# Kernel optimization log

Measured on AMD Instinct MI355X. Metric: run time of the kernel, lower is better.

Reference implementation:

```python
import jax, jax.numpy as jnp
import numpy as np
from jax import lax

B, S, MAXW, D, V, L = 32, 1024, 256, 512, 32000, 2


def setup_inputs() -> dict:
    key = jax.random.key(0)
    ks = jax.random.split(key, 10)
    x = jax.random.randint(ks[0], (B, S), 0, V)
    labels = jax.random.randint(ks[1], (B, MAXW), 0, 2)
    token_word_id = jnp.sort(
        jax.random.randint(ks[2], (B, S), 0, MAXW), axis=-1
    ).astype(jnp.int32)
    s = 1.0 / np.sqrt(D).astype(np.float32)
    emb = (jax.random.normal(ks[3], (V, D), dtype=jnp.float32) * 0.02).at[0].set(0.0)
    W_ih = jax.random.uniform(ks[4], (L, 4 * D, D), minval=-s, maxval=s, dtype=jnp.float32)
    W_hh = jax.random.uniform(ks[5], (L, 4 * D, D), minval=-s, maxval=s, dtype=jnp.float32)
    b_ih = jax.random.uniform(ks[6], (L, 4 * D), minval=-s, maxval=s, dtype=jnp.float32)
    b_hh = jax.random.uniform(ks[7], (L, 4 * D), minval=-s, maxval=s, dtype=jnp.float32)
    W_out = jax.random.uniform(ks[8], (2, D), minval=-s, maxval=s, dtype=jnp.float32)
    b_out = jax.random.uniform(ks[9], (2,), minval=-s, maxval=s, dtype=jnp.float32)
    return dict(x=x, labels=labels, token_word_id=token_word_id, emb=emb,
                W_ih=W_ih, W_hh=W_hh, b_ih=b_ih, b_hh=b_hh,
                W_out=W_out, b_out=b_out)


def _lstm_layer(xs, Wih, Whh, bih, bhh):
    # xs: [B, S, Din]; torch gate order: i, f, g, o
    H = Whh.shape[1]
    x_proj = jnp.einsum('bsd,gd->bsg', xs, Wih) + bih + bhh  # [B,S,4H]
    h0 = jnp.zeros((xs.shape[0], H), xs.dtype)
    c0 = jnp.zeros((xs.shape[0], H), xs.dtype)

    def step(carry, xt):
        h, c = carry
        gates = xt + h @ Whh.T
        i, f, g, o = jnp.split(gates, 4, axis=-1)
        i = jax.nn.sigmoid(i)
        f = jax.nn.sigmoid(f)
        g = jnp.tanh(g)
        o = jax.nn.sigmoid(o)
        c = f * c + i * g
        h = o * jnp.tanh(c)
        return (h, c), h

    _, hs = lax.scan(step, (h0, c0), x_proj.transpose(1, 0, 2))  # [S,B,H]
    return hs.transpose(1, 0, 2)


def reference(x, labels, token_word_id, emb, W_ih, W_hh, b_ih, b_hh, W_out, b_out):
    h = emb[x]  # [B,S,D]
    for l in range(L):
        h = _lstm_layer(h, W_ih[l], W_hh[l], b_ih[l], b_hh[l])
    # ragged token->word mean pooling (segment mean over flattened batch*word ids)
    seg = (jnp.arange(B, dtype=jnp.int32)[:, None] * MAXW + token_word_id).reshape(-1)
    flat = h.reshape(B * S, D)
    sums = jax.ops.segment_sum(flat, seg, num_segments=B * MAXW)
    cnts = jax.ops.segment_sum(jnp.ones((B * S,), h.dtype), seg, num_segments=B * MAXW)
    pooled = jnp.where(cnts[:, None] > 0, sums / jnp.maximum(cnts, 1.0)[:, None], 0.0)
    # span head (dropout is identity in eval)
    logits = pooled @ W_out.T + b_out            # [B*MAXW, 2]
    logp = jax.nn.log_softmax(logits, axis=-1)
    lab = labels.reshape(-1)
    loss = -jnp.mean(jnp.take_along_axis(logp, lab[:, None], axis=1))
    return logits, loss
```

## Files before the change

kernel.cpp:

```cpp
#include <hip/hip_runtime.h>
#include <hip/hip_fp16.h>

typedef unsigned short u16;
typedef unsigned int u32;
typedef unsigned long long u64;
typedef short s16x8 __attribute__((ext_vector_type(8)));
typedef float f32x4 __attribute__((ext_vector_type(4)));

#define BB   32
#define SS   1024
#define DD   512
#define G4   2048
#define MAXW 256
#define NWG  32
#define RING 8
#define HS   (BB*DD)

__device__ __forceinline__ u16 f2bf(float f){
  unsigned int u = __float_as_uint(f);
  u += 0x7fff + ((u >> 16) & 1);
  return (u16)(u >> 16);
}
__device__ __forceinline__ float bf2f(u16 h){
  return __uint_as_float(((unsigned int)h) << 16);
}
__device__ __forceinline__ float sigm(float x){ return 1.f/(1.f + __expf(-x)); }
__device__ __forceinline__ float ftanh(float x){
  float ax = fabsf(x);
  float e = __expf(-2.f*ax);
  float t = (1.f - e)/(1.f + e);
  return copysignf(t, x);
}

__global__ void k_prep(const float* __restrict__ Wih, const float* __restrict__ Whh,
                       const float* __restrict__ bih, const float* __restrict__ bhh,
                       u16* __restrict__ Wih_b, u16* __restrict__ Whh_b,
                       float* __restrict__ biasp){
  long i = (long)blockIdx.x*blockDim.x + threadIdx.x;
  long n = 2l*G4*DD;
  long stride = (long)gridDim.x*blockDim.x;
  for (long k = i; k < n; k += stride){
    Wih_b[k] = f2bf(Wih[k]);
    Whh_b[k] = f2bf(Whh[k]);
  }
  for (long k = i; k < 2*G4; k += stride){
    int lyr = (int)(k / G4), nn = (int)(k % G4);
    int col = nn >> 2, q = nn & 3;
    int g = q*DD + col;
    biasp[k] = bih[lyr*G4 + g] + bhh[lyr*G4 + g];
  }
}

__global__ void k_embed(const int* __restrict__ x, const float* __restrict__ emb,
                        u16* __restrict__ out){
  int bs = blockIdx.x;
  int tok = x[bs];
  const float* src = emb + (size_t)tok * DD;
  u16* dst = out + (size_t)bs * DD;
  for (int d = threadIdx.x; d < DD; d += blockDim.x) dst[d] = f2bf(src[d]);
}

__device__ __forceinline__ void wait2(const u32* p1, u32 n1,
                                      const u32* p2, u32 n2, int& budget){
  if (n1 == 0u && n2 == 0u) return;
  while (budget > 0){
    u32 v1 = n1 ? __hip_atomic_load(p1, __ATOMIC_RELAXED, __HIP_MEMORY_SCOPE_AGENT)
                : 0xffffffffu;
    u32 v2 = n2 ? __hip_atomic_load(p2, __ATOMIC_RELAXED, __HIP_MEMORY_SCOPE_AGENT)
                : 0xffffffffu;
    int ok = (v1 >= n1) && (v2 >= n2);
    if (__all(ok)) break;
    budget--;
    __builtin_amdgcn_s_sleep(1);
  }
}

__device__ __forceinline__ void stage_h(const u16* slab, char* lds, int tid){
  u64 d[16];
  #pragma unroll
  for (int j = 0; j < 16; j++)
    d[j] = __hip_atomic_load((const u64*)slab + j*256 + tid,
                             __ATOMIC_RELAXED, __HIP_MEMORY_SCOPE_AGENT);
  #pragma unroll
  for (int j = 0; j < 16; j++){
    int e = j*256 + tid;
    int b = e >> 7, c8 = e & 127;
    *(u64*)(lds + b*1024 + ((c8*8) ^ ((b & 7) << 4))) = d[j];
  }
}

#define FRAG_BYT(kk) ((lane & 15)*1024 + (((kk)*64 + (lane>>4)*16) ^ (((lane & 15) & 7) << 4)))

__global__ __launch_bounds__(256, 1) void k_recur2(
    const u16* __restrict__ h_io,
    const u16* __restrict__ Wih_b,
    const u16* __restrict__ Whh_b,
    const float* __restrict__ biasp,
    u16* __restrict__ h1r,
    u16* __restrict__ h2r,
    u32* __restrict__ flags,
    u16* __restrict__ h_seq2){
  __shared__ char hX[32768];
  __shared__ char hH[32768];
  const int tid = threadIdx.x;
  const int lane = tid & 63, wv = tid >> 6;
  const int wg = blockIdx.x;
  const bool isL2 = wg >= NWG;
  const int id = wg & (NWG - 1);

  u32* c1 = flags;
  u32* c2 = flags + 64;

  const int pa = id*64 + wv*16 + (lane & 15);
  const size_t arow = (size_t)((pa & 3)*DD + (pa >> 2))*DD;
  const int koff = (lane >> 4)*8;
  const size_t lyrOff = isL2 ? (size_t)G4*DD : 0;
  s16x8 ahh[16], aih[16];
  #pragma unroll
  for (int kk = 0; kk < 16; kk++){
    ahh[kk] = *(const s16x8*)(Whh_b + lyrOff + arow + kk*32 + koff);
    aih[kk] = *(const s16x8*)(Wih_b + lyrOff + arow + kk*32 + koff);
  }
  #pragma unroll
  for (int kk = 0; kk < 16; kk++){
    asm volatile("" : "+v"(ahh[kk]));
    asm volatile("" : "+v"(aih[kk]));
  }

  const int oc = id*16 + wv*4 + (lane >> 4);
  const int b0 = lane & 15, b1 = b0 + 16;
  const f32x4 b4 = *(const f32x4*)(biasp + (isL2 ? G4 : 0) + oc*4);
  float c0 = 0.f, cst1 = 0.f;
  int budget = 1 << 22;

  if (!isL2){
    for (int t = 0; t < SS; t++){
      u64 xd[16];
      #pragma unroll
      for (int j = 0; j < 16; j++){
        int e = j*256 + tid;
        xd[j] = *((const u64*)h_io + ((size_t)(e >> 7)*SS + t)*128 + (e & 127));
      }
      #pragma unroll
      for (int j = 0; j < 16; j++){
        int e = j*256 + tid;
        int b = e >> 7, c8 = e & 127;
        *(u64*)(hX + b*1024 + ((c8*8) ^ ((b & 7) << 4))) = xd[j];
      }
      __syncthreads();
      f32x4 e0 = {0.f,0.f,0.f,0.f}, e1 = {0.f,0.f,0.f,0.f};
      #pragma unroll
      for (int kk = 0; kk < 16; kk++){
        int byt = FRAG_BYT(kk);
        s16x8 f0 = *(const s16x8*)(hX + byt);
        s16x8 f1 = *(const s16x8*)(hX + byt + 16*1024);
        e0 = __builtin_amdgcn_mfma_f32_16x16x32_bf16(aih[kk], f0, e0, 0, 0, 0);
        e1 = __builtin_amdgcn_mfma_f32_16x16x32_bf16(aih[kk], f1, e1, 0, 0, 0);
      }
      u32 n1 = (t > 0) ? (u32)(NWG*t) : 0u;
      u32 n2 = (t >= RING) ? (u32)(NWG*(t - RING + 1)) : 0u;
      wait2(c1, n1, c2, n2, budget);
      if (t > 0){
        stage_h(h1r + (size_t)((t-1) & (RING-1))*HS, hH, tid);
        __syncthreads();
        #pragma unroll
        for (int kk = 0; kk < 16; kk++){
          int byt = FRAG_BYT(kk);
          s16x8 f0 = *(const s16x8*)(hH + byt);
          s16x8 f1 = *(const s16x8*)(hH + byt + 16*1024);
          e0 = __builtin_amdgcn_mfma_f32_16x16x32_bf16(ahh[kk], f0, e0, 0, 0, 0);
          e1 = __builtin_amdgcn_mfma_f32_16x16x32_bf16(ahh[kk], f1, e1, 0, 0, 0);
        }
      }
      float ig = sigm (e0[0] + b4[0]), fg = sigm (e0[1] + b4[1]);
      float gg = ftanh(e0[2] + b4[2]), og = sigm (e0[3] + b4[3]);
      c0 = fg*c0 + ig*gg;
      float hv0 = og * ftanh(c0);
      ig = sigm (e1[0] + b4[0]); fg = sigm (e1[1] + b4[1]);
      gg = ftanh(e1[2] + b4[2]); og = sigm (e1[3] + b4[3]);
      cst1 = fg*cst1 + ig*gg;
      float hv1 = og * ftanh(cst1);
      u16 hh0 = f2bf(hv0), hh1 = f2bf(hv1);
      u32 p0 = (u32)hh0 | (((u32)__shfl((int)hh0, (lane + 16) & 63) & 0xffffu) << 16);
      u32 p1 = (u32)hh1 | (((u32)__shfl((int)hh1, (lane + 16) & 63) & 0xffffu) << 16);
      u16* dst = h1r + (size_t)(t & (RING-1))*HS;
      if (((lane >> 4) & 1) == 0){
        __hip_atomic_store((u32*)(dst + (size_t)b0*DD + oc), p0,
                           __ATOMIC_RELAXED, __HIP_MEMORY_SCOPE_AGENT);
        __hip_atomic_store((u32*)(dst + (size_t)b1*DD + oc), p1,
                           __ATOMIC_RELAXED, __HIP_MEMORY_SCOPE_AGENT);
      }
      asm volatile("s_waitcnt vmcnt(0)" ::: "memory");
      __syncthreads();
      if (tid == 0) atomicAdd(c1, 1u);
    }
  } else {
    for (int t = 0; t < SS; t++){
      f32x4 e0 = {0.f,0.f,0.f,0.f}, e1 = {0.f,0.f,0.f,0.f};
      if (t > 0){
        wait2(c2, (u32)(NWG*t), c2, 0u, budget);
        stage_h(h2r + (size_t)((t-1) & 1)*HS, hH, tid);
        __syncthreads();
        #pragma unroll
        for (int kk = 0; kk < 16; kk++){
          int byt = FRAG_BYT(kk);
          s16x8 f0 = *(const s16x8*)(hH + byt);
          s16x8 f1 = *(const s16x8*)(hH + byt + 16*1024);
          e0 = __builtin_amdgcn_mfma_f32_16x16x32_bf16(ahh[kk], f0, e0, 0, 0, 0);
          e1 = __builtin_amdgcn_mfma_f32_16x16x32_bf16(ahh[kk], f1, e1, 0, 0, 0);
        }
      }
      wait2(c1, (u32)(NWG*(t+1)), c2, 0u, budget);
      stage_h(h1r + (size_t)(t & (RING-1))*HS, hX, tid);
      __syncthreads();
      #pragma unroll
      for (int kk = 0; kk < 16; kk++){
        int byt = FRAG_BYT(kk);
        s16x8 f0 = *(const s16x8*)(hX + byt);
        s16x8 f1 = *(const s16x8*)(hX + byt + 16*1024);
        e0 = __builtin_amdgcn_mfma_f32_16x16x32_bf16(aih[kk], f0, e0, 0, 0, 0);
        e1 = __builtin_amdgcn_mfma_f32_16x16x32_bf16(aih[kk], f1, e1, 0, 0, 0);
      }
      float ig = sigm (e0[0] + b4[0]), fg = sigm (e0[1] + b4[1]);
      float gg = ftanh(e0[2] + b4[2]), og = sigm (e0[3] + b4[3]);
      c0 = fg*c0 + ig*gg;
      float hv0 = og * ftanh(c0);
      ig = sigm (e1[0] + b4[0]); fg = sigm (e1[1] + b4[1]);
      gg = ftanh(e1[2] + b4[2]); og = sigm (e1[3] + b4[3]);
      cst1 = fg*cst1 + ig*gg;
      float hv1 = og * ftanh(cst1);
      u16 hh0 = f2bf(hv0), hh1 = f2bf(hv1);
      u32 p0 = (u32)hh0 | (((u32)__shfl((int)hh0, (lane + 16) & 63) & 0xffffu) << 16);
      u32 p1 = (u32)hh1 | (((u32)__shfl((int)hh1, (lane + 16) & 63) & 0xffffu) << 16);
      u16* dst = h2r + (size_t)(t & 1)*HS;
      if (((lane >> 4) & 1) == 0){
        __hip_atomic_store((u32*)(dst + (size_t)b0*DD + oc), p0,
                           __ATOMIC_RELAXED, __HIP_MEMORY_SCOPE_AGENT);
        __hip_atomic_store((u32*)(dst + (size_t)b1*DD + oc), p1,
                           __ATOMIC_RELAXED, __HIP_MEMORY_SCOPE_AGENT);
        *(u32*)(h_seq2 + ((size_t)b0*SS + t)*DD + oc) = p0;
        *(u32*)(h_seq2 + ((size_t)b1*SS + t)*DD + oc) = p1;
      }
      asm volatile("s_waitcnt vmcnt(0)" ::: "memory");
      __syncthreads();
      if (tid == 0) atomicAdd(c2, 1u);
    }
  }
}

__global__ __launch_bounds__(64) void k_pool(const u16* __restrict__ h_seq,
                                             const int* __restrict__ twid,
                                             const float* __restrict__ Wout,
                                             const float* __restrict__ bout,
                                             float* __restrict__ out){
  int bw = blockIdx.x;
  int b = bw >> 8, w = bw & 255;
  const int* tw = twid + b*SS;
  __shared__ int s_lo, s_hi;
  if (threadIdx.x == 0){
    int l = 0, r = SS;
    while (l < r){ int m = (l + r) >> 1; if (tw[m] < w) l = m + 1; else r = m; }
    s_lo = l;
    r = SS;
    while (l < r){ int m = (l + r) >> 1; if (tw[m] < w + 1) l = m + 1; else r = m; }
    s_hi = l;
  }
  __syncthreads();
  int lo = s_lo, hi = s_hi, cnt = hi - lo;
  int lane = threadIdx.x;
  float p0 = 0.f, p1 = 0.f;
  if (cnt > 0){
    float sum[8] = {0.f,0.f,0.f,0.f,0.f,0.f,0.f,0.f};
    for (int t = lo; t < hi; t++){
      const u16* hp = h_seq + ((size_t)b*SS + t)*DD + lane*8;
      int4 v = *(const int4*)hp;
      const u16* u = (const u16*)&v;
      #pragma unroll
      for (int j = 0; j < 8; j++) sum[j] += bf2f(u[j]);
    }
    float inv = 1.f/(float)cnt;
    #pragma unroll
    for (int j = 0; j < 8; j++){
      float pv = sum[j]*inv;
      int d = lane*8 + j;
      p0 += pv * Wout[d];
      p1 += pv * Wout[DD + d];
    }
  }
  #pragma unroll
  for (int off = 32; off; off >>= 1){
    p0 += __shfl_down(p0, off);
    p1 += __shfl_down(p1, off);
  }
  if (lane == 0){
    out[bw*2 + 0] = p0 + bout[0];
    out[bw*2 + 1] = p1 + bout[1];
  }
}

__global__ __launch_bounds__(256) void k_loss(const float* __restrict__ logits,
                                              const int* __restrict__ labels,
                                              float* __restrict__ out_loss){
  __shared__ float red[256];
  float acc = 0.f;
  for (int i = threadIdx.x; i < BB*MAXW; i += 256){
    float z0 = logits[i*2], z1 = logits[i*2 + 1];
    float m = fmaxf(z0, z1);
    float lse = m + __logf(__expf(z0 - m) + __expf(z1 - m));
    float zl = labels[i] ? z1 : z0;
    acc += (lse - zl);
  }
  red[threadIdx.x] = acc;
  __syncthreads();
  for (int s2 = 128; s2; s2 >>= 1){
    if (threadIdx.x < s2) red[threadIdx.x] += red[threadIdx.x + s2];
    __syncthreads();
  }
  if (threadIdx.x == 0) out_loss[0] = red[0] / (float)(BB*MAXW);
}

extern "C" void kernel_launch(void* const* d_in, const int* in_sizes, int n_in,
                              void* d_out, int out_size, void* d_ws, size_t ws_size,
                              hipStream_t stream){
  (void)in_sizes; (void)n_in; (void)out_size; (void)ws_size;
  const int*   x      = (const int*)  d_in[0];
  const int*   labels = (const int*)  d_in[1];
  const int*   twid   = (const int*)  d_in[2];
  const float* emb    = (const float*)d_in[3];
  const float* Wih    = (const float*)d_in[4];
  const float* Whh    = (const float*)d_in[5];
  const float* bih    = (const float*)d_in[6];
  const float* bhh    = (const float*)d_in[7];
  const float* Wout   = (const float*)d_in[8];
  const float* bout   = (const float*)d_in[9];
  float* out = (float*)d_out;

  char* ws = (char*)d_ws;
  size_t off = 0;
  u16*   h_io   = (u16*)  (ws + off); off += (size_t)BB*SS*DD*2;
  u16*   h_seq2 = (u16*)  (ws + off); off += (size_t)BB*SS*DD*2;
  u16*   Wih_b  = (u16*)  (ws + off); off += (size_t)2*G4*DD*2;
  u16*   Whh_b  = (u16*)  (ws + off); off += (size_t)2*G4*DD*2;
  float* biasp  = (float*)(ws + off); off += (size_t)2*G4*4;
  u16*   h1r    = (u16*)  (ws + off); off += (size_t)RING*HS*2;
  u16*   h2r    = (u16*)  (ws + off); off += (size_t)2*HS*2;
  u32*   flags  = (u32*)  (ws + off); off += 1024;

  k_prep<<<2048, 256, 0, stream>>>(Wih, Whh, bih, bhh, Wih_b, Whh_b, biasp);
  k_embed<<<BB*SS, 256, 0, stream>>>(x, emb, h_io);

  hipMemsetAsync(flags, 0, 1024, stream);

  k_recur2<<<2*NWG, 256, 0, stream>>>(h_io, Wih_b, Whh_b, biasp,
                                      h1r, h2r, flags, h_seq2);

  k_pool<<<BB*MAXW, 64, 0, stream>>>(h_seq2, twid, Wout, bout, out);
  k_loss<<<1, 256, 0, stream>>>(out, labels, out + BB*MAXW*2);
}
```

Baseline: 5.183 ms.

## Halve LSTM workgroups, double threads, tile hidden-state exchange layout and prefetch inputs

```diff
diff --git a/kernel.cpp b/kernel.cpp
--- a/kernel.cpp
+++ b/kernel.cpp
@@ -12,7 +12,7 @@
 #define DD   512
 #define G4   2048
 #define MAXW 256
-#define NWG  32
+#define NWG  16
 #define RING 8
 #define HS   (BB*DD)
 
@@ -75,23 +75,25 @@
   }
 }
 
-__device__ __forceinline__ void stage_h(const u16* slab, char* lds, int tid){
-  u64 d[16];
-  #pragma unroll
-  for (int j = 0; j < 16; j++)
-    d[j] = __hip_atomic_load((const u64*)slab + j*256 + tid,
+__device__ __forceinline__ void stage_tiled(const u16* slab, char* lds, int tid){
+  u64 d[8];
+  #pragma unroll
+  for (int j = 0; j < 8; j++)
+    d[j] = __hip_atomic_load((const u64*)slab + j*512 + tid,
                              __ATOMIC_RELAXED, __HIP_MEMORY_SCOPE_AGENT);
   #pragma unroll
-  for (int j = 0; j < 16; j++){
-    int e = j*256 + tid;
-    int b = e >> 7, c8 = e & 127;
-    *(u64*)(lds + b*1024 + ((c8*8) ^ ((b & 7) << 4))) = d[j];
+  for (int j = 0; j < 8; j++){
+    int e = j*512 + tid;
+    int tile = e >> 7, u = e & 127;
+    int b = u >> 2, c4 = u & 3;
+    int byt = tile*32 + c4*8;
+    *(u64*)(lds + b*1024 + (byt ^ ((b & 7) << 4))) = d[j];
   }
 }
 
 #define FRAG_BYT(kk) ((lane & 15)*1024 + (((kk)*64 + (lane>>4)*16) ^ (((lane & 15) & 7) << 4)))
 
-__global__ __launch_bounds__(256, 1) void k_recur2(
+__global__ __launch_bounds__(512, 1) void k_recur2(
     const u16* __restrict__ h_io,
     const u16* __restrict__ Wih_b,
     const u16* __restrict__ Whh_b,
@@ -111,7 +113,7 @@
   u32* c1 = flags;
   u32* c2 = flags + 64;
 
-  const int pa = id*64 + wv*16 + (lane & 15);
+  const int pa = id*128 + wv*16 + (lane & 15);
   const size_t arow = (size_t)((pa & 3)*DD + (pa >> 2))*DD;
   const int koff = (lane >> 4)*8;
   const size_t lyrOff = isL2 ? (size_t)G4*DD : 0;
@@ -127,23 +129,28 @@
     asm volatile("" : "+v"(aih[kk]));
   }
 
-  const int oc = id*16 + wv*4 + (lane >> 4);
+  const int oc = id*32 + wv*4 + (lane >> 4);
+  const int cl = wv*4 + (lane >> 4);
   const int b0 = lane & 15, b1 = b0 + 16;
   const f32x4 b4 = *(const f32x4*)(biasp + (isL2 ? G4 : 0) + oc*4);
   float c0 = 0.f, cst1 = 0.f;
   int budget = 1 << 22;
 
+  const int pk_tile = tid >> 8, pk_b = (tid >> 3) & 31, pk_cp = tid & 7;
+  const int pk_lds = pk_b*64 + pk_tile*32 + pk_cp*4;
+  const int pk_word = (id*2 + pk_tile)*256 + pk_b*8 + pk_cp;
+
   if (!isL2){
+    u64 xd[8];
+    #pragma unroll
+    for (int j = 0; j < 8; j++){
+      int e = j*512 + tid;
+      xd[j] = *((const u64*)h_io + ((size_t)(e >> 7)*SS + 0)*128 + (e & 127));
+    }
     for (int t = 0; t < SS; t++){
-      u64 xd[16];
       #pragma unroll
-      for (int j = 0; j < 16; j++){
-        int e = j*256 + tid;
-        xd[j] = *((const u64*)h_io + ((size_t)(e >> 7)*SS + t)*128 + (e & 127));
-      }
-      #pragma unroll
-      for (int j = 0; j < 16; j++){
-        int e = j*256 + tid;
+      for (int j = 0; j < 8; j++){
+        int e = j*512 + tid;
         int b = e >> 7, c8 = e & 127;
         *(u64*)(hX + b*1024 + ((c8*8) ^ ((b & 7) << 4))) = xd[j];
       }
@@ -161,7 +168,7 @@
       u32 n2 = (t >= RING) ? (u32)(NWG*(t - RING + 1)) : 0u;
       wait2(c1, n1, c2, n2, budget);
       if (t > 0){
-        stage_h(h1r + (size_t)((t-1) & (RING-1))*HS, hH, tid);
+        stage_tiled(h1r + (size_t)((t-1) & (RING-1))*HS, hH, tid);
         __syncthreads();
         #pragma unroll
         for (int kk = 0; kk < 16; kk++){
@@ -181,15 +188,20 @@
       cst1 = fg*cst1 + ig*gg;
       float hv1 = og * ftanh(cst1);
       u16 hh0 = f2bf(hv0), hh1 = f2bf(hv1);
-      u32 p0 = (u32)hh0 | (((u32)__shfl((int)hh0, (lane + 16) & 63) & 0xffffu) << 16);
-      u32 p1 = (u32)hh1 | (((u32)__shfl((int)hh1, (lane + 16) & 63) & 0xffffu) << 16);
-      u16* dst = h1r + (size_t)(t & (RING-1))*HS;
-      if (((lane >> 4) & 1) == 0){
-        __hip_atomic_store((u32*)(dst + (size_t)b0*DD + oc), p0,
-                           __ATOMIC_RELAXED, __HIP_MEMORY_SCOPE_AGENT);
-        __hip_atomic_store((u32*)(dst + (size_t)b1*DD + oc), p1,
-                           __ATOMIC_RELAXED, __HIP_MEMORY_SCOPE_AGENT);
-      }
+      if (t + 1 < SS){
+        #pragma unroll
+        for (int j = 0; j < 8; j++){
+          int e = j*512 + tid;
+          xd[j] = *((const u64*)h_io + ((size_t)(e >> 7)*SS + (t+1))*128 + (e & 127));
+        }
+      }
+      __syncthreads();
+      *(u16*)(hX + b0*64 + cl*2) = hh0;
+      *(u16*)(hX + b1*64 + cl*2) = hh1;
+      __syncthreads();
+      u32 wrd = *(u32*)(hX + pk_lds);
+      __hip_atomic_store((u32*)h1r + (size_t)(t & (RING-1))*(HS/2) + pk_word,
+                         wrd, __ATOMIC_RELAXED, __HIP_MEMORY_SCOPE_AGENT);
       asm volatile("s_waitcnt vmcnt(0)" ::: "memory");
       __syncthreads();
       if (tid == 0) atomicAdd(c1, 1u);
@@ -199,7 +211,7 @@
       f32x4 e0 = {0.f,0.f,0.f,0.f}, e1 = {0.f,0.f,0.f,0.f};
       if (t > 0){
         wait2(c2, (u32)(NWG*t), c2, 0u, budget);
-        stage_h(h2r + (size_t)((t-1) & 1)*HS, hH, tid);
+        stage_tiled(h2r + (size_t)((t-1) & 1)*HS, hH, tid);
         __syncthreads();
         #pragma unroll
         for (int kk = 0; kk < 16; kk++){
@@ -211,7 +223,7 @@
         }
       }
       wait2(c1, (u32)(NWG*(t+1)), c2, 0u, budget);
-      stage_h(h1r + (size_t)(t & (RING-1))*HS, hX, tid);
+      stage_tiled(h1r + (size_t)(t & (RING-1))*HS, hX, tid);
       __syncthreads();
       #pragma unroll
       for (int kk = 0; kk < 16; kk++){
@@ -230,17 +242,14 @@
       cst1 = fg*cst1 + ig*gg;
       float hv1 = og * ftanh(cst1);
       u16 hh0 = f2bf(hv0), hh1 = f2bf(hv1);
-      u32 p0 = (u32)hh0 | (((u32)__shfl((int)hh0, (lane + 16) & 63) & 0xffffu) << 16);
-      u32 p1 = (u32)hh1 | (((u32)__shfl((int)hh1, (lane + 16) & 63) & 0xffffu) << 16);
-      u16* dst = h2r + (size_t)(t & 1)*HS;
-      if (((lane >> 4) & 1) == 0){
-        __hip_atomic_store((u32*)(dst + (size_t)b0*DD + oc), p0,
-                           __ATOMIC_RELAXED, __HIP_MEMORY_SCOPE_AGENT);
-        __hip_atomic_store((u32*)(dst + (size_t)b1*DD + oc), p1,
-                           __ATOMIC_RELAXED, __HIP_MEMORY_SCOPE_AGENT);
-        *(u32*)(h_seq2 + ((size_t)b0*SS + t)*DD + oc) = p0;
-        *(u32*)(h_seq2 + ((size_t)b1*SS + t)*DD + oc) = p1;
-      }
+      __syncthreads();
+      *(u16*)(hX + b0*64 + cl*2) = hh0;
+      *(u16*)(hX + b1*64 + cl*2) = hh1;
+      __syncthreads();
+      u32 wrd = *(u32*)(hX + pk_lds);
+      __hip_atomic_store((u32*)h2r + (size_t)(t & 1)*(HS/2) + pk_word,
+                         wrd, __ATOMIC_RELAXED, __HIP_MEMORY_SCOPE_AGENT);
+      *((u32*)h_seq2 + (size_t)t*(HS/2) + pk_word) = wrd;
       asm volatile("s_waitcnt vmcnt(0)" ::: "memory");
       __syncthreads();
       if (tid == 0) atomicAdd(c2, 1u);
@@ -270,10 +279,11 @@
   int lane = threadIdx.x;
   float p0 = 0.f, p1 = 0.f;
   if (cnt > 0){
+    const char* hs = (const char*)h_seq;
+    const size_t lo_off = (size_t)(lane >> 1)*1024 + (size_t)b*32 + (lane & 1)*16;
     float sum[8] = {0.f,0.f,0.f,0.f,0.f,0.f,0.f,0.f};
     for (int t = lo; t < hi; t++){
-      const u16* hp = h_seq + ((size_t)b*SS + t)*DD + lane*8;
-      int4 v = *(const int4*)hp;
+      int4 v = *(const int4*)(hs + (size_t)t*32768 + lo_off);
       const u16* u = (const u16*)&v;
       #pragma unroll
       for (int j = 0; j < 8; j++) sum[j] += bf2f(u[j]);
@@ -351,7 +361,7 @@
 
   hipMemsetAsync(flags, 0, 1024, stream);
 
-  k_recur2<<<2*NWG, 256, 0, stream>>>(h_io, Wih_b, Whh_b, biasp,
+  k_recur2<<<2*NWG, 512, 0, stream>>>(h_io, Wih_b, Whh_b, biasp,
                                       h1r, h2r, flags, h_seq2);
 
   k_pool<<<BB*MAXW, 64, 0, stream>>>(h_seq2, twid, Wout, bout, out);
```

Measured after the change: 6.391 ms. +23.3%, slower.

## Prefetch next-step inputs and issue recurrent loads early in persistent LSTM

Applied to the files above, without the earlier changes.

```diff
diff --git a/kernel.cpp b/kernel.cpp
--- a/kernel.cpp
+++ b/kernel.cpp
@@ -31,6 +31,12 @@
   float t = (1.f - e)/(1.f + e);
   return copysignf(t, x);
 }
+
+#define BAR_LDS() { asm volatile("s_waitcnt lgkmcnt(0)" ::: "memory"); \
+                    __builtin_amdgcn_sched_barrier(0); \
+                    __builtin_amdgcn_s_barrier(); }
+#define VMDRAIN(n) { asm volatile("s_waitcnt vmcnt(" #n ")" ::: "memory"); \
+                     __builtin_amdgcn_sched_barrier(0); }
 
 __global__ void k_prep(const float* __restrict__ Wih, const float* __restrict__ Whh,
                        const float* __restrict__ bih, const float* __restrict__ bhh,
@@ -75,12 +81,7 @@
   }
 }
 
-__device__ __forceinline__ void stage_h(const u16* slab, char* lds, int tid){
-  u64 d[16];
-  #pragma unroll
-  for (int j = 0; j < 16; j++)
-    d[j] = __hip_atomic_load((const u64*)slab + j*256 + tid,
-                             __ATOMIC_RELAXED, __HIP_MEMORY_SCOPE_AGENT);
+__device__ __forceinline__ void lds_write16(char* lds, int tid, const u64* d){
   #pragma unroll
   for (int j = 0; j < 16; j++){
     int e = j*256 + tid;
@@ -134,20 +135,26 @@
   int budget = 1 << 22;
 
   if (!isL2){
+    u64 xd[16];
+    #pragma unroll
+    for (int j = 0; j < 16; j++){
+      int e = j*256 + tid;
+      xd[j] = *((const u64*)h_io + ((size_t)(e >> 7)*SS + 0)*128 + (e & 127));
+    }
     for (int t = 0; t < SS; t++){
-      u64 xd[16];
-      #pragma unroll
-      for (int j = 0; j < 16; j++){
-        int e = j*256 + tid;
-        xd[j] = *((const u64*)h_io + ((size_t)(e >> 7)*SS + t)*128 + (e & 127));
-      }
-      #pragma unroll
-      for (int j = 0; j < 16; j++){
-        int e = j*256 + tid;
-        int b = e >> 7, c8 = e & 127;
-        *(u64*)(hX + b*1024 + ((c8*8) ^ ((b & 7) << 4))) = xd[j];
-      }
-      __syncthreads();
+      u32 n1 = (t > 0) ? (u32)(NWG*t) : 0u;
+      u32 n2 = (t >= RING) ? (u32)(NWG*(t - RING + 1)) : 0u;
+      wait2(c1, n1, c2, n2, budget);
+      u64 d1[16];
+      if (t > 0){
+        const u64* s = (const u64*)(h1r + (size_t)((t-1) & (RING-1))*HS);
+        #pragma unroll
+        for (int j = 0; j < 16; j++)
+          d1[j] = __hip_atomic_load(s + j*256 + tid,
+                                    __ATOMIC_RELAXED, __HIP_MEMORY_SCOPE_AGENT);
+      }
+      lds_write16(hX, tid, xd);
+      BAR_LDS();
       f32x4 e0 = {0.f,0.f,0.f,0.f}, e1 = {0.f,0.f,0.f,0.f};
       #pragma unroll
       for (int kk = 0; kk < 16; kk++){
@@ -157,12 +164,9 @@
         e0 = __builtin_amdgcn_mfma_f32_16x16x32_bf16(aih[kk], f0, e0, 0, 0, 0);
         e1 = __builtin_amdgcn_mfma_f32_16x16x32_bf16(aih[kk], f1, e1, 0, 0, 0);
       }
-      u32 n1 = (t > 0) ? (u32)(NWG*t) : 0u;
-      u32 n2 = (t >= RING) ? (u32)(NWG*(t - RING + 1)) : 0u;
-      wait2(c1, n1, c2, n2, budget);
       if (t > 0){
-        stage_h(h1r + (size_t)((t-1) & (RING-1))*HS, hH, tid);
-        __syncthreads();
+        lds_write16(hH, tid, d1);
+        BAR_LDS();
         #pragma unroll
         for (int kk = 0; kk < 16; kk++){
           int byt = FRAG_BYT(kk);
@@ -190,17 +194,41 @@
         __hip_atomic_store((u32*)(dst + (size_t)b1*DD + oc), p1,
                            __ATOMIC_RELAXED, __HIP_MEMORY_SCOPE_AGENT);
       }
-      asm volatile("s_waitcnt vmcnt(0)" ::: "memory");
-      __syncthreads();
+      if (t + 1 < SS){
+        #pragma unroll
+        for (int j = 0; j < 16; j++){
+          int e = j*256 + tid;
+          xd[j] = *((const u64*)h_io + ((size_t)(e >> 7)*SS + (t+1))*128 + (e & 127));
+        }
+        VMDRAIN(16);
+      } else {
+        VMDRAIN(0);
+      }
+      __builtin_amdgcn_s_barrier();
       if (tid == 0) atomicAdd(c1, 1u);
     }
   } else {
     for (int t = 0; t < SS; t++){
+      wait2(c1, (u32)(NWG*(t+1)), c2, 0u, budget);
+      u64 d1[16];
+      {
+        const u64* s = (const u64*)(h1r + (size_t)(t & (RING-1))*HS);
+        #pragma unroll
+        for (int j = 0; j < 16; j++)
+          d1[j] = __hip_atomic_load(s + j*256 + tid,
+                                    __ATOMIC_RELAXED, __HIP_MEMORY_SCOPE_AGENT);
+      }
       f32x4 e0 = {0.f,0.f,0.f,0.f}, e1 = {0.f,0.f,0.f,0.f};
       if (t > 0){
         wait2(c2, (u32)(NWG*t), c2, 0u, budget);
-        stage_h(h2r + (size_t)((t-1) & 1)*HS, hH, tid);
-        __syncthreads();
+        u64 d2[16];
+        const u64* s2 = (const u64*)(h2r + (size_t)((t-1) & 1)*HS);
+        #pragma unroll
+        for (int j = 0; j < 16; j++)
+          d2[j] = __hip_atomic_load(s2 + j*256 + tid,
+                                    __ATOMIC_RELAXED, __HIP_MEMORY_SCOPE_AGENT);
+        lds_write16(hH, tid, d2);
+        BAR_LDS();
         #pragma unroll
         for (int kk = 0; kk < 16; kk++){
           int byt = FRAG_BYT(kk);
@@ -210,9 +238,8 @@
           e1 = __builtin_amdgcn_mfma_f32_16x16x32_bf16(ahh[kk], f1, e1, 0, 0, 0);
         }
       }
-      wait2(c1, (u32)(NWG*(t+1)), c2, 0u, budget);
-      stage_h(h1r + (size_t)(t & (RING-1))*HS, hX, tid);
-      __syncthreads();
+      lds_write16(hX, tid, d1);
+      BAR_LDS();
       #pragma unroll
       for (int kk = 0; kk < 16; kk++){
         int byt = FRAG_BYT(kk);
@@ -241,8 +268,8 @@
         *(u32*)(h_seq2 + ((size_t)b0*SS + t)*DD + oc) = p0;
         *(u32*)(h_seq2 + ((size_t)b1*SS + t)*DD + oc) = p1;
       }
-      asm volatile("s_waitcnt vmcnt(0)" ::: "memory");
-      __syncthreads();
+      VMDRAIN(0);
+      __builtin_amdgcn_s_barrier();
       if (tid == 0) atomicAdd(c2, 1u);
     }
   }
```

Measured after the change: 7.388 ms. +42.5%, slower.

## Merge layer-2 waits and preload both h slabs; move h_seq2 stores off critical path

Applied to the files above, without the earlier changes.

```diff
diff --git a/kernel.cpp b/kernel.cpp
--- a/kernel.cpp
+++ b/kernel.cpp
@@ -81,6 +81,15 @@
   for (int j = 0; j < 16; j++)
     d[j] = __hip_atomic_load((const u64*)slab + j*256 + tid,
                              __ATOMIC_RELAXED, __HIP_MEMORY_SCOPE_AGENT);
+  #pragma unroll
+  for (int j = 0; j < 16; j++){
+    int e = j*256 + tid;
+    int b = e >> 7, c8 = e & 127;
+    *(u64*)(lds + b*1024 + ((c8*8) ^ ((b & 7) << 4))) = d[j];
+  }
+}
+
+__device__ __forceinline__ void lds_write16(char* lds, int tid, const u64* d){
   #pragma unroll
   for (int j = 0; j < 16; j++){
     int e = j*256 + tid;
@@ -128,6 +137,7 @@
   }
 
   const int oc = id*16 + wv*4 + (lane >> 4);
+  const int cl = wv*4 + (lane >> 4);
   const int b0 = lane & 15, b1 = b0 + 16;
   const f32x4 b4 = *(const f32x4*)(biasp + (isL2 ? G4 : 0) + oc*4);
   float c0 = 0.f, cst1 = 0.f;
@@ -141,12 +151,7 @@
         int e = j*256 + tid;
         xd[j] = *((const u64*)h_io + ((size_t)(e >> 7)*SS + t)*128 + (e & 127));
       }
-      #pragma unroll
-      for (int j = 0; j < 16; j++){
-        int e = j*256 + tid;
-        int b = e >> 7, c8 = e & 127;
-        *(u64*)(hX + b*1024 + ((c8*8) ^ ((b & 7) << 4))) = xd[j];
-      }
+      lds_write16(hX, tid, xd);
       __syncthreads();
       f32x4 e0 = {0.f,0.f,0.f,0.f}, e1 = {0.f,0.f,0.f,0.f};
       #pragma unroll
@@ -196,10 +201,25 @@
     }
   } else {
     for (int t = 0; t < SS; t++){
+      wait2(c1, (u32)(NWG*(t+1)), c2, (t > 0) ? (u32)(NWG*t) : 0u, budget);
+      u64 d2[16], d1[16];
+      if (t > 0){
+        const u64* s2 = (const u64*)(h2r + (size_t)((t-1) & 1)*HS);
+        #pragma unroll
+        for (int j = 0; j < 16; j++)
+          d2[j] = __hip_atomic_load(s2 + j*256 + tid,
+                                    __ATOMIC_RELAXED, __HIP_MEMORY_SCOPE_AGENT);
+      }
+      {
+        const u64* s1 = (const u64*)(h1r + (size_t)(t & (RING-1))*HS);
+        #pragma unroll
+        for (int j = 0; j < 16; j++)
+          d1[j] = __hip_atomic_load(s1 + j*256 + tid,
+                                    __ATOMIC_RELAXED, __HIP_MEMORY_SCOPE_AGENT);
+      }
       f32x4 e0 = {0.f,0.f,0.f,0.f}, e1 = {0.f,0.f,0.f,0.f};
       if (t > 0){
-        wait2(c2, (u32)(NWG*t), c2, 0u, budget);
-        stage_h(h2r + (size_t)((t-1) & 1)*HS, hH, tid);
+        lds_write16(hH, tid, d2);
         __syncthreads();
         #pragma unroll
         for (int kk = 0; kk < 16; kk++){
@@ -210,8 +230,7 @@
           e1 = __builtin_amdgcn_mfma_f32_16x16x32_bf16(ahh[kk], f1, e1, 0, 0, 0);
         }
       }
-      wait2(c1, (u32)(NWG*(t+1)), c2, 0u, budget);
-      stage_h(h1r + (size_t)(t & (RING-1))*HS, hX, tid);
+      lds_write16(hX, tid, d1);
       __syncthreads();
       #pragma unroll
       for (int kk = 0; kk < 16; kk++){
@@ -238,12 +257,15 @@
                            __ATOMIC_RELAXED, __HIP_MEMORY_SCOPE_AGENT);
         __hip_atomic_store((u32*)(dst + (size_t)b1*DD + oc), p1,
                            __ATOMIC_RELAXED, __HIP_MEMORY_SCOPE_AGENT);
-        *(u32*)(h_seq2 + ((size_t)b0*SS + t)*DD + oc) = p0;
-        *(u32*)(h_seq2 + ((size_t)b1*SS + t)*DD + oc) = p1;
       }
       asm volatile("s_waitcnt vmcnt(0)" ::: "memory");
       __syncthreads();
       if (tid == 0) atomicAdd(c2, 1u);
+      if (((lane >> 4) & 1) == 0){
+        u32* hs = (u32*)h_seq2 + (size_t)t*(HS/2) + id*256;
+        hs[b0*8 + (cl >> 1)] = p0;
+        hs[b1*8 + (cl >> 1)] = p1;
+      }
     }
   }
 }
@@ -270,10 +292,11 @@
   int lane = threadIdx.x;
   float p0 = 0.f, p1 = 0.f;
   if (cnt > 0){
+    const char* hs = (const char*)h_seq;
+    const size_t lo_off = (size_t)(lane >> 1)*1024 + (size_t)b*32 + (lane & 1)*16;
     float sum[8] = {0.f,0.f,0.f,0.f,0.f,0.f,0.f,0.f};
     for (int t = lo; t < hi; t++){
-      const u16* hp = h_seq + ((size_t)b*SS + t)*DD + lane*8;
-      int4 v = *(const int4*)hp;
+      int4 v = *(const int4*)(hs + (size_t)t*32768 + lo_off);
       const u16* u = (const u16*)&v;
       #pragma unroll
       for (int j = 0; j < 8; j++) sum[j] += bf2f(u[j]);
```

Result: faster. 5.029 ms (-3.0%).
